# Kernel tuning notes

Measured on AMD Instinct MI355X. Metric: run time of the kernel, lower is better.

Reference implementation:

```python
import jax, jax.numpy as jnp
import numpy as np

N_NODES = 50000
N_EDGES = 1600000
IN_FEAT = 256
OUT_FEAT = 64


def setup_inputs() -> dict:
    key = jax.random.key(0)
    k1, k2, k3, k4, k5, k6 = jax.random.split(key, 6)
    feat = jax.random.normal(k1, (N_NODES, IN_FEAT), dtype=jnp.float32)
    edge_src = jax.random.randint(k2, (N_EDGES,), 0, N_NODES, dtype=jnp.int32)
    edge_dst = jax.random.randint(k3, (N_EDGES,), 0, N_NODES, dtype=jnp.int32)
    edge_weight = jax.random.uniform(k4, (N_EDGES,), dtype=jnp.float32)
    # Xavier-uniform init as in reset_parameters
    bound = float(np.sqrt(6.0 / (IN_FEAT + OUT_FEAT)))
    W_self = jax.random.uniform(k5, (IN_FEAT, OUT_FEAT), minval=-bound, maxval=bound, dtype=jnp.float32)
    W_neigh = jax.random.uniform(k6, (IN_FEAT, OUT_FEAT), minval=-bound, maxval=bound, dtype=jnp.float32)
    return {"feat": feat, "edge_src": edge_src, "edge_dst": edge_dst,
            "edge_weight": edge_weight, "W_self": W_self, "W_neigh": W_neigh}


def reference(feat, edge_src, edge_dst, edge_weight, W_self, W_neigh):
    # neigh_feat = spmm(adj, feat): row dst aggregates weighted neighbors src
    gathered = feat[edge_src] * edge_weight[:, None]          # [E, in_feat]
    neigh_feat = jax.ops.segment_sum(gathered, edge_dst, num_segments=N_NODES)  # [N, in_feat]
    self_feat = feat @ W_self                                 # [N, out_feat]
    neigh_feat = neigh_feat @ W_neigh                         # [N, out_feat]
    out = jax.nn.relu(self_feat + neigh_feat)
    # dropout p=0.0 -> identity
    return out
```

## Files before the change

### kernel.cpp

```cpp
#include <hip/hip_runtime.h>

#define IN_FEAT 256
#define OUT_FEAT 64
#define BBITS 5
#define BSZ 32
#define CAP_SLICE 256
#define CAP_BUCKET 1600
#define CNT_STRIDE 16

typedef __attribute__((ext_vector_type(8))) short bf16x8;
typedef __attribute__((ext_vector_type(4))) float f32x4;

static __device__ __forceinline__ short f2bf(float f) {
    unsigned u = __float_as_uint(f);
    unsigned r = (u + 0x7FFFu + ((u >> 16) & 1u)) >> 16;
    return (short)r;
}
static __device__ __forceinline__ float bflo(unsigned v) {
    return __uint_as_float(v << 16);
}
static __device__ __forceinline__ float bfhi(unsigned v) {
    return __uint_as_float(v & 0xFFFF0000u);
}

__global__ __launch_bounds__(256) void prep(
    const float* __restrict__ Wself,
    const float* __restrict__ Wneigh,
    bf16x8* __restrict__ Wfrag,
    int* __restrict__ cnt, int cnt_words)
{
    const int t = blockIdx.x * 256 + threadIdx.x;
    if (t < 4096) {
        const int kstep = t >> 9;
        const int ntile = (t >> 6) & 7;
        const int lane  = t & 63;
        const int quad  = lane >> 4;
        const int n     = ntile * 16 + (lane & 15);
        const float* src = (n < OUT_FEAT) ? (Wself + n) : (Wneigh + (n - OUT_FEAT));
        const int k0 = kstep * 32 + quad * 8;
        bf16x8 v;
#pragma unroll
        for (int j = 0; j < 8; ++j) v[j] = f2bf(src[(size_t)(k0 + j) * OUT_FEAT]);
        Wfrag[t] = v;
    }
    const int nthr = gridDim.x * 256;
    for (int i = t; i < cnt_words; i += nthr) cnt[i] = 0;
}

__global__ __launch_bounds__(256) void gemm_scatter(
    const float* __restrict__ feat,
    const bf16x8* __restrict__ Wfrag,
    unsigned short* __restrict__ accSelf,
    unsigned short* __restrict__ Pn,
    const int* __restrict__ esrc,
    const int* __restrict__ edst,
    const float* __restrict__ ew,
    int* __restrict__ cnt,
    unsigned* __restrict__ binned,
    int n_nodes, int n_edges, int NB)
{
    const int wave = threadIdx.x >> 6;
    const int lane = threadIdx.x & 63;

    if (wave < 2) {
        const int row0 = (blockIdx.x * 2 + wave) * 16;
        if (row0 < n_nodes) {
            const int quad = lane >> 4;
            const int l15  = lane & 15;

            f32x4 c[8];
#pragma unroll
            for (int i = 0; i < 8; ++i) c[i] = (f32x4){0.f, 0.f, 0.f, 0.f};

            const int arow = min(row0 + l15, n_nodes - 1);
            const float* afeat = feat + (size_t)arow * IN_FEAT + quad * 8;

#pragma unroll
            for (int kstep = 0; kstep < 8; ++kstep) {
                const float4 x = *(const float4*)(afeat + kstep * 32);
                const float4 y = *(const float4*)(afeat + kstep * 32 + 4);
                bf16x8 a;
                a[0] = f2bf(x.x); a[1] = f2bf(x.y); a[2] = f2bf(x.z); a[3] = f2bf(x.w);
                a[4] = f2bf(y.x); a[5] = f2bf(y.y); a[6] = f2bf(y.z); a[7] = f2bf(y.w);
                bf16x8 b[8];
#pragma unroll
                for (int nt = 0; nt < 8; ++nt) b[nt] = Wfrag[(kstep * 8 + nt) * 64 + lane];
#pragma unroll
                for (int nt = 0; nt < 8; ++nt)
                    c[nt] = __builtin_amdgcn_mfma_f32_16x16x32_bf16(a, b[nt], c[nt], 0, 0, 0);
            }

#pragma unroll
            for (int nt = 0; nt < 8; ++nt) {
                unsigned short* dst = (nt < 4) ? accSelf : Pn;
                const int col = (nt & 3) * 16 + l15;
#pragma unroll
                for (int r = 0; r < 4; ++r) {
                    const int row = row0 + quad * 4 + r;
                    if (row < n_nodes)
                        dst[(size_t)row * OUT_FEAT + col] = (unsigned short)f2bf(c[nt][r]);
                }
            }
        }
    }

    {
        const long base  = (long)blockIdx.x * 1024;
        const int slice = blockIdx.x & 7;
        int d[4], pos[4];
        unsigned rec[4];
        bool ok[4];
#pragma unroll
        for (int k = 0; k < 4; ++k) {
            const long idx = base + k * 256 + (int)threadIdx.x;
            ok[k] = idx < n_edges;
            if (ok[k]) {
                d[k] = edst[idx];
                const unsigned s  = (unsigned)esrc[idx];
                const unsigned wq = (unsigned)__float2int_rn(ew[idx] * 2047.0f);
                rec[k] = ((unsigned)(d[k] & (BSZ - 1)) << 27) | (wq << 16) | s;
            }
        }
#pragma unroll
        for (int k = 0; k < 4; ++k)
            if (ok[k]) pos[k] = atomicAdd(&cnt[((size_t)slice * NB + (d[k] >> BBITS)) * CNT_STRIDE], 1);
#pragma unroll
        for (int k = 0; k < 4; ++k)
            if (ok[k] && pos[k] < CAP_SLICE)
                binned[((size_t)slice * NB + (d[k] >> BBITS)) * CAP_SLICE + pos[k]] = rec[k];
    }
}

__global__ __launch_bounds__(256) void bucket_gather(
    const unsigned* __restrict__ binned,
    const int* __restrict__ cnt,
    const unsigned short* __restrict__ Pn,
    const unsigned short* __restrict__ accSelf,
    float* __restrict__ out, int n_nodes, int NB)
{
    __shared__ unsigned raw[8 * CAP_SLICE];
    __shared__ int2 sepk[CAP_BUCKET];
    __shared__ int  scnt[8];
    __shared__ int  hcnt[BSZ];
    __shared__ int  hoff[BSZ + 1];
    __shared__ int  hcur[BSZ];

    const int b = blockIdx.x;
    const int t = threadIdx.x;

    if (t < 8) scnt[t] = min(cnt[((size_t)t * NB + b) * CNT_STRIDE], CAP_SLICE);
    if (t < BSZ) hcnt[t] = 0;
    __syncthreads();

#pragma unroll
    for (int sl = 0; sl < 8; ++sl) {
        const int nrec4 = (scnt[sl] + 3) >> 2;
        const uint4* rb4 = (const uint4*)(binned + ((size_t)sl * NB + b) * CAP_SLICE);
        uint4* rw4 = (uint4*)(raw + sl * CAP_SLICE);
        for (int i = t; i < nrec4; i += 256) rw4[i] = rb4[i];
    }
    __syncthreads();

#pragma unroll
    for (int sl = 0; sl < 8; ++sl) {
        const int nrec = scnt[sl];
        const unsigned* rw = raw + sl * CAP_SLICE;
        for (int i = t; i < nrec; i += 256)
            atomicAdd(&hcnt[rw[i] >> 27], 1);
    }
    __syncthreads();
    if (t == 0) {
        int run = 0;
#pragma unroll
        for (int k = 0; k < BSZ; ++k) { hoff[k] = run; run += hcnt[k]; }
        hoff[BSZ] = run;
    }
    __syncthreads();
    if (t < BSZ) hcur[t] = hoff[t];
    __syncthreads();

#pragma unroll
    for (int sl = 0; sl < 8; ++sl) {
        const int nrec = scnt[sl];
        const unsigned* rw = raw + sl * CAP_SLICE;
        for (int i = t; i < nrec; i += 256) {
            const unsigned p = rw[i];
            const int pos = atomicAdd(&hcur[p >> 27], 1);
            if (pos < CAP_BUCKET) {
                const float w = (float)((p >> 16) & 0x7FFu) * (1.0f / 2047.0f);
                sepk[pos] = make_int2((int)(p & 0xFFFFu), __float_as_int(w));
            }
        }
    }
    __syncthreads();

    const int wv   = t >> 6;
    const int lane = t & 63;
    const int half = lane >> 5;
    const int c2   = (lane & 31) * 2;

#pragma unroll
    for (int ldn = wv * 8; ldn < wv * 8 + 8; ++ldn) {
        const int dst = b * BSZ + ldn;
        if (dst >= n_nodes) break;
        const int beg = min(hoff[ldn], CAP_BUCKET);
        const int end = min(hoff[ldn + 1], CAP_BUCKET);

        float a0 = 0.f, a1 = 0.f, b0 = 0.f, b1 = 0.f;
        float g0 = 0.f, g1 = 0.f, h0 = 0.f, h1 = 0.f;
        int e = beg + half;
        for (; e + 6 < end; e += 8) {
            const int2 p0 = sepk[e + 0];
            const int2 p1 = sepk[e + 2];
            const int2 p2 = sepk[e + 4];
            const int2 p3 = sepk[e + 6];
            const unsigned v0 = *(const unsigned*)(Pn + (size_t)p0.x * OUT_FEAT + c2);
            const unsigned v1 = *(const unsigned*)(Pn + (size_t)p1.x * OUT_FEAT + c2);
            const unsigned v2 = *(const unsigned*)(Pn + (size_t)p2.x * OUT_FEAT + c2);
            const unsigned v3 = *(const unsigned*)(Pn + (size_t)p3.x * OUT_FEAT + c2);
            const float w0 = __int_as_float(p0.y);
            const float w1 = __int_as_float(p1.y);
            const float w2 = __int_as_float(p2.y);
            const float w3 = __int_as_float(p3.y);
            a0 += w0 * bflo(v0); a1 += w0 * bfhi(v0);
            b0 += w1 * bflo(v1); b1 += w1 * bfhi(v1);
            g0 += w2 * bflo(v2); g1 += w2 * bfhi(v2);
            h0 += w3 * bflo(v3); h1 += w3 * bfhi(v3);
        }
        for (; e < end; e += 2) {
            const int2 p = sepk[e];
            const unsigned v = *(const unsigned*)(Pn + (size_t)p.x * OUT_FEAT + c2);
            const float w = __int_as_float(p.y);
            a0 += w * bflo(v); a1 += w * bfhi(v);
        }
        float s0 = (a0 + b0) + (g0 + h0);
        float s1 = (a1 + b1) + (g1 + h1);
        s0 += __shfl_xor(s0, 32, 64);
        s1 += __shfl_xor(s1, 32, 64);
        if (half == 0) {
            const unsigned sv = *(const unsigned*)(accSelf + (size_t)dst * OUT_FEAT + c2);
            float2 o;
            o.x = fmaxf(bflo(sv) + s0, 0.f);
            o.y = fmaxf(bfhi(sv) + s1, 0.f);
            *(float2*)(out + (size_t)dst * OUT_FEAT + c2) = o;
        }
    }
}

extern "C" void kernel_launch(void* const* d_in, const int* in_sizes, int n_in,
                              void* d_out, int out_size, void* d_ws, size_t ws_size,
                              hipStream_t stream) {
    const float* feat   = (const float*)d_in[0];
    const int*   esrc   = (const int*)  d_in[1];
    const int*   edst   = (const int*)  d_in[2];
    const float* ew     = (const float*)d_in[3];
    const float* Wself  = (const float*)d_in[4];
    const float* Wneigh = (const float*)d_in[5];

    const int n_nodes = in_sizes[0] / IN_FEAT;
    const int n_edges = in_sizes[1];
    const int NB = (n_nodes + BSZ - 1) / BSZ;

    bf16x8* Wfrag           = (bf16x8*)d_ws;
    unsigned short* accSelf = (unsigned short*)((char*)d_ws + 65536);
    unsigned short* Pn      = accSelf + (size_t)n_nodes * OUT_FEAT;
    unsigned* binned = (unsigned*)(Pn + (size_t)n_nodes * OUT_FEAT);
    int*   cnt     = (int*)(binned + (size_t)8 * NB * CAP_SLICE);
    float* out     = (float*)d_out;

    const int cnt_words = 8 * NB * CNT_STRIDE;
    prep<<<64, 256, 0, stream>>>(Wself, Wneigh, Wfrag, cnt, cnt_words);

    const int sblocks = (n_edges + 1023) / 1024;
    const int tblocks = ((n_nodes + 15) / 16 + 1) / 2;
    const int fblocks = (sblocks > tblocks) ? sblocks : tblocks;
    gemm_scatter<<<fblocks, 256, 0, stream>>>(
        feat, Wfrag, accSelf, Pn, esrc, edst, ew, cnt, binned, n_nodes, n_edges, NB);

    bucket_gather<<<NB, 256, 0, stream>>>(binned, cnt, Pn, accSelf, out, n_nodes, NB);
}
```

Measured before the change: 205.7 us.

## Overlap edge binning atomics with GEMM and fuse histogram into bucket load

In the fused GEMM+scatter kernel, the edge loads and atomic slot reservations now run before the MFMA GEMM, and the binned stores come after it, so atomic latency can hide behind the GEMM. The GEMM work moves from two waves in every block to all four waves in every even block. In bucket_gather the per-destination histogram atomics are folded into the global-to-LDS copy loop, which removes one barrier and one extra LDS pass. The risks are that odd blocks sit idle during the GEMM phase, and that the GEMM accumulator registers stay live alongside the edge registers, which may raise register pressure.

```diff
diff --git a/kernel.cpp b/kernel.cpp
--- a/kernel.cpp
+++ b/kernel.cpp
@@ -62,8 +62,29 @@
     const int wave = threadIdx.x >> 6;
     const int lane = threadIdx.x & 63;
 
-    if (wave < 2) {
-        const int row0 = (blockIdx.x * 2 + wave) * 16;
+    const long base  = (long)blockIdx.x * 1024;
+    const int slice = blockIdx.x & 7;
+    int bin[4], pos[4];
+    unsigned rec[4];
+    bool ok[4];
+#pragma unroll
+    for (int k = 0; k < 4; ++k) {
+        const long idx = base + k * 256 + (int)threadIdx.x;
+        ok[k] = idx < n_edges;
+        if (ok[k]) {
+            const int d = edst[idx];
+            const unsigned s  = (unsigned)esrc[idx];
+            const unsigned wq = (unsigned)__float2int_rn(ew[idx] * 2047.0f);
+            bin[k] = d >> BBITS;
+            rec[k] = ((unsigned)(d & (BSZ - 1)) << 27) | (wq << 16) | s;
+        }
+    }
+#pragma unroll
+    for (int k = 0; k < 4; ++k)
+        if (ok[k]) pos[k] = atomicAdd(&cnt[((size_t)slice * NB + bin[k]) * CNT_STRIDE], 1);
+
+    if ((blockIdx.x & 1) == 0) {
+        const int row0 = ((blockIdx.x >> 1) * 4 + wave) * 16;
         if (row0 < n_nodes) {
             const int quad = lane >> 4;
             const int l15  = lane & 15;
@@ -104,31 +125,10 @@
         }
     }
 
-    {
-        const long base  = (long)blockIdx.x * 1024;
-        const int slice = blockIdx.x & 7;
-        int d[4], pos[4];
-        unsigned rec[4];
-        bool ok[4];
-#pragma unroll
-        for (int k = 0; k < 4; ++k) {
-            const long idx = base + k * 256 + (int)threadIdx.x;
-            ok[k] = idx < n_edges;
-            if (ok[k]) {
-                d[k] = edst[idx];
-                const unsigned s  = (unsigned)esrc[idx];
-                const unsigned wq = (unsigned)__float2int_rn(ew[idx] * 2047.0f);
-                rec[k] = ((unsigned)(d[k] & (BSZ - 1)) << 27) | (wq << 16) | s;
-            }
-        }
-#pragma unroll
-        for (int k = 0; k < 4; ++k)
-            if (ok[k]) pos[k] = atomicAdd(&cnt[((size_t)slice * NB + (d[k] >> BBITS)) * CNT_STRIDE], 1);
-#pragma unroll
-        for (int k = 0; k < 4; ++k)
-            if (ok[k] && pos[k] < CAP_SLICE)
-                binned[((size_t)slice * NB + (d[k] >> BBITS)) * CAP_SLICE + pos[k]] = rec[k];
-    }
+#pragma unroll
+    for (int k = 0; k < 4; ++k)
+        if (ok[k] && pos[k] < CAP_SLICE)
+            binned[((size_t)slice * NB + bin[k]) * CAP_SLICE + pos[k]] = rec[k];
 }
 
 __global__ __launch_bounds__(256) void bucket_gather(
@@ -154,19 +154,19 @@
 
 #pragma unroll
     for (int sl = 0; sl < 8; ++sl) {
-        const int nrec4 = (scnt[sl] + 3) >> 2;
+        const int nrec  = scnt[sl];
+        const int nrec4 = (nrec + 3) >> 2;
         const uint4* rb4 = (const uint4*)(binned + ((size_t)sl * NB + b) * CAP_SLICE);
         uint4* rw4 = (uint4*)(raw + sl * CAP_SLICE);
-        for (int i = t; i < nrec4; i += 256) rw4[i] = rb4[i];
-    }
-    __syncthreads();
-
-#pragma unroll
-    for (int sl = 0; sl < 8; ++sl) {
-        const int nrec = scnt[sl];
-        const unsigned* rw = raw + sl * CAP_SLICE;
-        for (int i = t; i < nrec; i += 256)
-            atomicAdd(&hcnt[rw[i] >> 27], 1);
+        for (int i = t; i < nrec4; i += 256) {
+            const uint4 v = rb4[i];
+            rw4[i] = v;
+            const int e0 = i * 4;
+            if (e0 + 0 < nrec) atomicAdd(&hcnt[v.x >> 27], 1);
+            if (e0 + 1 < nrec) atomicAdd(&hcnt[v.y >> 27], 1);
+            if (e0 + 2 < nrec) atomicAdd(&hcnt[v.z >> 27], 1);
+            if (e0 + 3 < nrec) atomicAdd(&hcnt[v.w >> 27], 1);
+        }
     }
     __syncthreads();
     if (t == 0) {
@@ -272,7 +272,7 @@
     prep<<<64, 256, 0, stream>>>(Wself, Wneigh, Wfrag, cnt, cnt_words);
 
     const int sblocks = (n_edges + 1023) / 1024;
-    const int tblocks = ((n_nodes + 15) / 16 + 1) / 2;
+    const int tblocks = 2 * ((n_nodes + 63) / 64);
     const int fblocks = (sblocks > tblocks) ? sblocks : tblocks;
     gemm_scatter<<<fblocks, 256, 0, stream>>>(
         feat, Wfrag, accSelf, Pn, esrc, edst, ew, cnt, binned, n_nodes, n_edges, NB);
```

Result: slower. 221.9 us (+7.9%).
